# Kernel optimization log

Hardware: AMD Instinct MI355X
Metric: run time of the kernel (lower is better)

Reference implementation:

```python
import jax, jax.numpy as jnp
import numpy as np

EMBED_DIM, KQ_DIM, V_DIM = 512, 64, 64
B, S = 2, 4096

def setup_inputs() -> dict:
    key = jax.random.key(0)
    k1, k2, k3, k4 = jax.random.split(key, 4)
    X = jax.random.normal(k1, (B, S, EMBED_DIM), dtype=jnp.float32)
    # nn.Linear(in, out, bias=False) weight has shape (out, in); y = x @ W.T
    Wq = jax.random.normal(k2, (KQ_DIM, EMBED_DIM), dtype=jnp.float32) * (EMBED_DIM ** -0.5)
    Wk = jax.random.normal(k3, (KQ_DIM, EMBED_DIM), dtype=jnp.float32) * (EMBED_DIM ** -0.5)
    Wv = jax.random.normal(k4, (V_DIM, EMBED_DIM), dtype=jnp.float32) * (EMBED_DIM ** -0.5)
    return {"X": X, "Wq": Wq, "Wk": Wk, "Wv": Wv}

def reference(X, Wq, Wk, Wv):
    # Q,K: [B,S,kq], V: [B,S,v]
    Q = jnp.einsum('bse,ke->bsk', X, Wq)
    K = jnp.einsum('bse,ke->bsk', X, Wk)
    V = jnp.einsum('bse,ve->bsv', X, Wv)
    scores = jnp.einsum('bqk,bsk->bqs', Q, K)  # [B,S,S]
    # FAITHFUL quirk: original divides by kq_dim**(-0.5) == multiply by sqrt(kq_dim)
    scaled = scores / (KQ_DIM ** -0.5)
    attn = jax.nn.softmax(scaled, axis=-1)
    context = jnp.einsum('bqs,bsv->bqv', attn, V)  # [B,S,v]
    return context
```

## Files before the change

### kernel.cpp

```cpp
#include <hip/hip_runtime.h>
#include <hip/hip_bf16.h>


typedef float  f32x16 __attribute__((ext_vector_type(16)));
typedef short  v8bf   __attribute__((ext_vector_type(8)));
typedef int    v4i    __attribute__((ext_vector_type(4)));

#define MFMA32(a, b, c) __builtin_amdgcn_mfma_f32_32x32x16_bf16((a), (b), (c), 0, 0, 0)

union Frag { v4i i4; v8bf b8; unsigned u[4]; };

__device__ __forceinline__ unsigned short f2bf(float x) {
    unsigned u = __float_as_uint(x);
    return (unsigned short)((u + 0x7fffu + ((u >> 16) & 1u)) >> 16);
}
__device__ __forceinline__ float bf2f(unsigned short h) {
    return __uint_as_float(((unsigned)h) << 16);
}
__device__ __forceinline__ unsigned cvt_pk_bf16(float a, float b) {
    unsigned r;
    asm("v_cvt_pk_bf16_f32 %0, %1, %2" : "=v"(r) : "v"(a), "v"(b));
    return r;
}


__global__ __launch_bounds__(256) void splitW_kernel(
    const float* __restrict__ wq, const float* __restrict__ wk, const float* __restrict__ wv,
    unsigned short* __restrict__ hi, unsigned short* __restrict__ lo)
{
    int i = blockIdx.x * 256 + threadIdx.x;
    int e = i * 4;
    const float* src = (e < 32768) ? wq : (e < 65536) ? wk : wv;
    const float sc = (e < 32768) ? 11.541560327111707f : 1.0f;
    int off = e & 32767;
    float4 v = *reinterpret_cast<const float4*>(src + off);
    v.x *= sc; v.y *= sc; v.z *= sc; v.w *= sc;
    unsigned short h0 = f2bf(v.x), h1 = f2bf(v.y), h2 = f2bf(v.z), h3 = f2bf(v.w);
    unsigned short l0 = f2bf(v.x - bf2f(h0)), l1 = f2bf(v.y - bf2f(h1));
    unsigned short l2 = f2bf(v.z - bf2f(h2)), l3 = f2bf(v.w - bf2f(h3));
    reinterpret_cast<uint2*>(hi)[i] =
        make_uint2((unsigned)h0 | ((unsigned)h1 << 16), (unsigned)h2 | ((unsigned)h3 << 16));
    reinterpret_cast<uint2*>(lo)[i] =
        make_uint2((unsigned)l0 | ((unsigned)l1 << 16), (unsigned)l2 | ((unsigned)l3 << 16));
}


__global__ __launch_bounds__(384, 1) void proj_kernel(
    const float* __restrict__ X,
    const unsigned short* __restrict__ Whi, const unsigned short* __restrict__ Wlo,
    unsigned short* __restrict__ Qhi, unsigned short* __restrict__ Qlo,
    unsigned short* __restrict__ Khi, unsigned short* __restrict__ Klo,
    unsigned short* __restrict__ VT)
{
    __shared__ uint4 XhiS[2048];
    __shared__ uint4 XloS[2048];
    __shared__ float t4[4][32][33];

    const int tid = threadIdx.x;
    const int w = tid >> 6;
    const int l = tid & 63, h = l >> 5, r32 = l & 31;
    const int row0 = blockIdx.x * 32;
    const int g = w >> 1, ct = w & 1;

    for (int id = tid; id < 2048; id += 384) {
        const int row = id >> 6, cc = id & 63;
        const float* xp = X + (row0 + row) * 512 + cc * 8;
        float4 va = *reinterpret_cast<const float4*>(xp);
        float4 vb = *reinterpret_cast<const float4*>(xp + 4);
        float xs[8] = {va.x, va.y, va.z, va.w, vb.x, vb.y, vb.z, vb.w};
        unsigned uh[4], ul[4];
#pragma unroll
        for (int j = 0; j < 4; ++j) {
            unsigned short h0 = f2bf(xs[2 * j]),            h1 = f2bf(xs[2 * j + 1]);
            unsigned short l0 = f2bf(xs[2 * j] - bf2f(h0)), l1 = f2bf(xs[2 * j + 1] - bf2f(h1));
            uh[j] = (unsigned)h0 | ((unsigned)h1 << 16);
            ul[j] = (unsigned)l0 | ((unsigned)l1 << 16);
        }
        const int idx = row * 64 + (cc ^ (row & 7));
        XhiS[idx] = make_uint4(uh[0], uh[1], uh[2], uh[3]);
        XloS[idx] = make_uint4(ul[0], ul[1], ul[2], ul[3]);
    }
    __syncthreads();

    f32x16 a0;
#pragma unroll
    for (int r = 0; r < 16; ++r) a0[r] = 0.f;

    for (int kc = 0; kc < 32; ++kc) {
        const int k0 = kc * 16 + 8 * h;
        const int idx = r32 * 64 + ((kc * 2 + h) ^ (r32 & 7));
        Frag xh, b0h;
        xh.i4 = *reinterpret_cast<const v4i*>(&XhiS[idx]);
        const int w0 = (g * 64 + ct * 32 + r32) * 512 + k0;
        b0h.i4 = *reinterpret_cast<const v4i*>(Whi + w0);
        a0 = MFMA32(xh.b8, b0h.b8, a0);
        if (g < 2) {
            Frag xl, b0l;
            xl.i4 = *reinterpret_cast<const v4i*>(&XloS[idx]);
            b0l.i4 = *reinterpret_cast<const v4i*>(Wlo + w0);
            a0 = MFMA32(xh.b8, b0l.b8, a0);
            a0 = MFMA32(xl.b8, b0h.b8, a0);
        }
    }

    const int bb = row0 >> 12;
    const int tl = (row0 & 4095) >> 5;

    if (g < 2) {
#pragma unroll
        for (int u = 0; u < 16; ++u)
            t4[w][(u & 3) + 8 * (u >> 2) + 4 * h][r32] = a0[u];
    }
    __syncthreads();

    if (g == 2) {
#pragma unroll
        for (int c = 0; c < 2; ++c)
#pragma unroll
            for (int hp = 0; hp < 2; ++hp) {
                unsigned p0 = (unsigned)f2bf(a0[8*c + 4*hp + 0]) |
                              ((unsigned)f2bf(a0[8*c + 4*hp + 1]) << 16);
                unsigned p1 = (unsigned)f2bf(a0[8*c + 4*hp + 2]) |
                              ((unsigned)f2bf(a0[8*c + 4*hp + 3]) << 16);
                const int off = ((((bb*128 + tl)*2 + c)*2 + ct)*64 + 32*hp + r32)*8 + 4*h;
                *reinterpret_cast<uint2*>(VT + off) = make_uint2(p0, p1);
            }
    } else if (g == 0) {
        unsigned wh[8], wl[8];
#pragma unroll
        for (int j = 0; j < 8; ++j) {
            float x0 = t4[w][r32][16 * h + 2 * j];
            float x1 = t4[w][r32][16 * h + 2 * j + 1];
            unsigned short h0 = f2bf(x0), h1 = f2bf(x1);
            unsigned short l0 = f2bf(x0 - bf2f(h0)), l1 = f2bf(x1 - bf2f(h1));
            wh[j] = (unsigned)h0 | ((unsigned)h1 << 16);
            wl[j] = (unsigned)l0 | ((unsigned)l1 << 16);
        }
        const int off = (row0 + r32) * 64 + ct * 32 + 16 * h;
        *reinterpret_cast<uint4*>(Qhi + off)     = make_uint4(wh[0], wh[1], wh[2], wh[3]);
        *reinterpret_cast<uint4*>(Qhi + off + 8) = make_uint4(wh[4], wh[5], wh[6], wh[7]);
        *reinterpret_cast<uint4*>(Qlo + off)     = make_uint4(wl[0], wl[1], wl[2], wl[3]);
        *reinterpret_cast<uint4*>(Qlo + off + 8) = make_uint4(wl[4], wl[5], wl[6], wl[7]);
    } else {
        const int dc = ct * 2 + h;
#pragma unroll
        for (int hp = 0; hp < 2; ++hp) {
            unsigned wh[4], wl[4];
#pragma unroll
            for (int jj = 0; jj < 4; ++jj) {
                float x0 = t4[w][r32][16 * h + 8 * hp + 2 * jj];
                float x1 = t4[w][r32][16 * h + 8 * hp + 2 * jj + 1];
                unsigned short h0 = f2bf(x0), h1 = f2bf(x1);
                unsigned short l0 = f2bf(x0 - bf2f(h0)), l1 = f2bf(x1 - bf2f(h1));
                wh[jj] = (unsigned)h0 | ((unsigned)h1 << 16);
                wl[jj] = (unsigned)l0 | ((unsigned)l1 << 16);
            }
            const int off = (((bb*128 + tl)*4 + dc)*64 + 32*hp + r32)*8;
            *reinterpret_cast<uint4*>(Khi + off) = make_uint4(wh[0], wh[1], wh[2], wh[3]);
            *reinterpret_cast<uint4*>(Klo + off) = make_uint4(wl[0], wl[1], wl[2], wl[3]);
        }
    }
}


__global__ __launch_bounds__(256, 3) void attn_kernel(
    const unsigned short* __restrict__ Qhi, const unsigned short* __restrict__ Qlo,
    const unsigned short* __restrict__ Khi, const unsigned short* __restrict__ Klo,
    const unsigned short* __restrict__ VT,
    float* __restrict__ Opart, float* __restrict__ ml)
{
    __shared__ unsigned char RAW[49152];
    auto S  = reinterpret_cast<unsigned short(*)[3][4096]>(RAW);
    auto sO = reinterpret_cast<float(*)[32][68]>(RAW);

    const int tid = threadIdx.x;
    const int w = tid >> 6;
    const int l = tid & 63;
    const int h = l >> 5;
    const int q = l & 31;
    const int bx = blockIdx.x;
    const int b  = bx >> 5;
    const int ks = blockIdx.y;
    const int rowg0 = bx * 128 + w * 32;

    Frag qh[4], ql[4];
#pragma unroll
    for (int dc = 0; dc < 4; ++dc) {
        const int o = (rowg0 + q) * 64 + dc * 16 + 8 * h;
        qh[dc].i4 = *reinterpret_cast<const v4i*>(Qhi + o);
        ql[dc].i4 = *reinterpret_cast<const v4i*>(Qlo + o);
    }

    f32x16 o0, o1;
#pragma unroll
    for (int r = 0; r < 16; ++r) { o0[r] = 0.f; o1[r] = 0.f; }
    float m_run = -1e30f, l_run = 0.f;

    const size_t tb0 = ((size_t)(b * 128 + ks * 16)) * 2048;

    uint4 rgA0, rgA1, rgB0, rgB1, rgC0, rgC1;
    {
        const size_t s = tb0 + (size_t)tid * 8;
        rgA0 = *reinterpret_cast<const uint4*>(Khi + s);
        rgA1 = *reinterpret_cast<const uint4*>(Khi + s + 2048);
        rgB0 = *reinterpret_cast<const uint4*>(Klo + s);
        rgB1 = *reinterpret_cast<const uint4*>(Klo + s + 2048);
        rgC0 = *reinterpret_cast<const uint4*>(VT + s);
        rgC1 = *reinterpret_cast<const uint4*>(VT + s + 2048);
        *reinterpret_cast<uint4*>(&S[0][0][tid * 8])        = rgA0;
        *reinterpret_cast<uint4*>(&S[0][0][tid * 8 + 2048]) = rgA1;
        *reinterpret_cast<uint4*>(&S[0][1][tid * 8])        = rgB0;
        *reinterpret_cast<uint4*>(&S[0][1][tid * 8 + 2048]) = rgB1;
        *reinterpret_cast<uint4*>(&S[0][2][tid * 8])        = rgC0;
        *reinterpret_cast<uint4*>(&S[0][2][tid * 8 + 2048]) = rgC1;
    }
    __syncthreads();

    for (int it = 0; it < 8; ++it) {
        const int cur = it & 1;
        if (it < 7) {
            const size_t s = tb0 + (size_t)(it + 1) * 4096 + (size_t)tid * 8;
            rgA0 = *reinterpret_cast<const uint4*>(Khi + s);
            rgA1 = *reinterpret_cast<const uint4*>(Khi + s + 2048);
            rgB0 = *reinterpret_cast<const uint4*>(Klo + s);
            rgB1 = *reinterpret_cast<const uint4*>(Klo + s + 2048);
            rgC0 = *reinterpret_cast<const uint4*>(VT + s);
            rgC1 = *reinterpret_cast<const uint4*>(VT + s + 2048);
        }

        f32x16 sA, sB;
#pragma unroll
        for (int r = 0; r < 16; ++r) { sA[r] = 0.f; sB[r] = 0.f; }
#pragma unroll
        for (int dc = 0; dc < 4; ++dc) {
            Frag kha, kla, khb, klb;
            kha.i4 = *reinterpret_cast<const v4i*>(&S[cur][0][dc * 512 + l * 8]);
            khb.i4 = *reinterpret_cast<const v4i*>(&S[cur][0][2048 + dc * 512 + l * 8]);
            kla.i4 = *reinterpret_cast<const v4i*>(&S[cur][1][dc * 512 + l * 8]);
            klb.i4 = *reinterpret_cast<const v4i*>(&S[cur][1][2048 + dc * 512 + l * 8]);
            sA = MFMA32(kha.b8, qh[dc].b8, sA);
            sB = MFMA32(khb.b8, qh[dc].b8, sB);
            sA = MFMA32(kha.b8, ql[dc].b8, sA);
            sB = MFMA32(khb.b8, ql[dc].b8, sB);
            sA = MFMA32(kla.b8, qh[dc].b8, sA);
            sB = MFMA32(klb.b8, qh[dc].b8, sB);
        }

        float mb;
        {
            float t[8];
#pragma unroll
            for (int jj = 0; jj < 4; ++jj) {
                t[jj]     = fmaxf(fmaxf(sA[4 * jj], sA[4 * jj + 1]),
                                  fmaxf(sA[4 * jj + 2], sA[4 * jj + 3]));
                t[4 + jj] = fmaxf(fmaxf(sB[4 * jj], sB[4 * jj + 1]),
                                  fmaxf(sB[4 * jj + 2], sB[4 * jj + 3]));
            }
            float u0 = fmaxf(fmaxf(t[0], t[1]), fmaxf(t[2], t[3]));
            float u1 = fmaxf(fmaxf(t[4], t[5]), fmaxf(t[6], t[7]));
            mb = fmaxf(u0, u1);
        }
        mb = fmaxf(mb, __shfl_xor(mb, 32));

        if (!__all(mb <= m_run + 8.f)) {
            const float m_new = fmaxf(m_run, mb);
            const float f = exp2f(m_run - m_new);
#pragma unroll
            for (int r = 0; r < 16; ++r) { o0[r] *= f; o1[r] *= f; }
            l_run *= f;
            m_run = m_new;
        }

        float p[32];
        float ps0 = 0.f, ps1 = 0.f, ps2 = 0.f, ps3 = 0.f;
#pragma unroll
        for (int r = 0; r < 16; r += 4) {
            p[r]      = exp2f(sA[r]     - m_run); ps0 += p[r];
            p[r + 1]  = exp2f(sA[r + 1] - m_run); ps1 += p[r + 1];
            p[r + 2]  = exp2f(sA[r + 2] - m_run); ps2 += p[r + 2];
            p[r + 3]  = exp2f(sA[r + 3] - m_run); ps3 += p[r + 3];
            p[16 + r]     = exp2f(sB[r]     - m_run); ps0 += p[16 + r];
            p[16 + r + 1] = exp2f(sB[r + 1] - m_run); ps1 += p[16 + r + 1];
            p[16 + r + 2] = exp2f(sB[r + 2] - m_run); ps2 += p[16 + r + 2];
            p[16 + r + 3] = exp2f(sB[r + 3] - m_run); ps3 += p[16 + r + 3];
        }
        float ps = (ps0 + ps1) + (ps2 + ps3);
        ps += __shfl_xor(ps, 32);
        l_run += ps;

        unsigned U[16];
#pragma unroll
        for (int j = 0; j < 8; ++j) {
            U[j]     = cvt_pk_bf16(p[2 * j],      p[2 * j + 1]);
            U[8 + j] = cvt_pk_bf16(p[16 + 2 * j], p[16 + 2 * j + 1]);
        }
        unsigned tA0 = h ? U[0]  : U[2];
        unsigned tA1 = h ? U[1]  : U[3];
        unsigned tA2 = h ? U[4]  : U[6];
        unsigned tA3 = h ? U[5]  : U[7];
        unsigned tB0 = h ? U[8]  : U[10];
        unsigned tB1 = h ? U[9]  : U[11];
        unsigned tB2 = h ? U[12] : U[14];
        unsigned tB3 = h ? U[13] : U[15];
        unsigned rA0 = __shfl_xor(tA0, 32);
        unsigned rA1 = __shfl_xor(tA1, 32);
        unsigned rA2 = __shfl_xor(tA2, 32);
        unsigned rA3 = __shfl_xor(tA3, 32);
        unsigned rB0 = __shfl_xor(tB0, 32);
        unsigned rB1 = __shfl_xor(tB1, 32);
        unsigned rB2 = __shfl_xor(tB2, 32);
        unsigned rB3 = __shfl_xor(tB3, 32);
        Frag p0f, p1f, p2f, p3f;
        if (h == 0) {
            p0f.u[0] = U[0];  p0f.u[1] = U[1];  p0f.u[2] = rA0;   p0f.u[3] = rA1;
            p1f.u[0] = U[4];  p1f.u[1] = U[5];  p1f.u[2] = rA2;   p1f.u[3] = rA3;
            p2f.u[0] = U[8];  p2f.u[1] = U[9];  p2f.u[2] = rB0;   p2f.u[3] = rB1;
            p3f.u[0] = U[12]; p3f.u[1] = U[13]; p3f.u[2] = rB2;   p3f.u[3] = rB3;
        } else {
            p0f.u[0] = rA0;   p0f.u[1] = rA1;   p0f.u[2] = U[2];  p0f.u[3] = U[3];
            p1f.u[0] = rA2;   p1f.u[1] = rA3;   p1f.u[2] = U[6];  p1f.u[3] = U[7];
            p2f.u[0] = rB0;   p2f.u[1] = rB1;   p2f.u[2] = U[10]; p2f.u[3] = U[11];
            p3f.u[0] = rB2;   p3f.u[1] = rB3;   p3f.u[2] = U[14]; p3f.u[3] = U[15];
        }

#pragma unroll
        for (int tb = 0; tb < 2; ++tb) {
#pragma unroll
            for (int c = 0; c < 2; ++c) {
                const Frag& pf = tb ? (c ? p3f : p2f) : (c ? p1f : p0f);
#pragma unroll
                for (int vc = 0; vc < 2; ++vc) {
                    Frag vf;
                    vf.i4 = *reinterpret_cast<const v4i*>(
                        &S[cur][2][tb * 2048 + (c * 2 + vc) * 512 + l * 8]);
                    if (vc == 0) o0 = MFMA32(vf.b8, pf.b8, o0);
                    else         o1 = MFMA32(vf.b8, pf.b8, o1);
                }
            }
        }

        if (it < 7) {
            const int nxt = cur ^ 1;
            *reinterpret_cast<uint4*>(&S[nxt][0][tid * 8])        = rgA0;
            *reinterpret_cast<uint4*>(&S[nxt][0][tid * 8 + 2048]) = rgA1;
            *reinterpret_cast<uint4*>(&S[nxt][1][tid * 8])        = rgB0;
            *reinterpret_cast<uint4*>(&S[nxt][1][tid * 8 + 2048]) = rgB1;
            *reinterpret_cast<uint4*>(&S[nxt][2][tid * 8])        = rgC0;
            *reinterpret_cast<uint4*>(&S[nxt][2][tid * 8 + 2048]) = rgC1;
        }
        __syncthreads();
    }

    if (h == 0) {
        const int rowg = rowg0 + q;
        *reinterpret_cast<float2*>(&ml[((size_t)ks * 8192 + rowg) * 2]) =
            make_float2(m_run, l_run);
    }
#pragma unroll
    for (int vc = 0; vc < 2; ++vc) {
        const f32x16& a = vc ? o1 : o0;
#pragma unroll
        for (int u = 0; u < 4; ++u) {
            float4 v4 = make_float4(a[4 * u], a[4 * u + 1], a[4 * u + 2], a[4 * u + 3]);
            *reinterpret_cast<float4*>(&sO[w][q][vc * 32 + 8 * u + 4 * h]) = v4;
        }
    }
    __syncthreads();

#pragma unroll
    for (int k = 0; k < 8; ++k) {
        const int f = tid + k * 256;
        const int rl = f >> 4;
        const int v4 = f & 15;
        float4 val = *reinterpret_cast<const float4*>(&sO[rl >> 5][rl & 31][v4 * 4]);
        *reinterpret_cast<float4*>(
            &Opart[(((size_t)ks * 8192) + bx * 128 + rl) * 64 + v4 * 4]) = val;
    }
}

__global__ __launch_bounds__(256) void merge_kernel(
    const float* __restrict__ Opart, const float* __restrict__ ml, float* __restrict__ out)
{
    const int idx = blockIdx.x * 256 + threadIdx.x;
    const int row = idx >> 4, vb = (idx & 15) * 4;
    float mv[8], lv[8];
    float ms = -1e30f;
#pragma unroll
    for (int s = 0; s < 8; ++s) {
        float2 m2 = *reinterpret_cast<const float2*>(&ml[((size_t)s * 8192 + row) * 2]);
        mv[s] = m2.x; lv[s] = m2.y;
        ms = fmaxf(ms, m2.x);
    }
    float L = 0.f;
    float a0 = 0.f, a1 = 0.f, a2 = 0.f, a3 = 0.f;
#pragma unroll
    for (int s = 0; s < 8; ++s) {
        const float fw = exp2f(mv[s] - ms);
        L += fw * lv[s];
        float4 a = *reinterpret_cast<const float4*>(
            &Opart[((size_t)s * 8192 + row) * 64 + vb]);
        a0 += fw * a.x; a1 += fw * a.y; a2 += fw * a.z; a3 += fw * a.w;
    }
    const float inv = 1.0f / L;
    *reinterpret_cast<float4*>(out + (size_t)row * 64 + vb) =
        make_float4(a0 * inv, a1 * inv, a2 * inv, a3 * inv);
}


extern "C" void kernel_launch(void* const* d_in, const int* in_sizes, int n_in,
                              void* d_out, int out_size, void* d_ws, size_t ws_size,
                              hipStream_t stream)
{
    const float* X  = (const float*)d_in[0];
    const float* Wq = (const float*)d_in[1];
    const float* Wk = (const float*)d_in[2];
    const float* Wv = (const float*)d_in[3];
    float* out = (float*)d_out;

    unsigned short* Qhi = (unsigned short*)d_ws;
    unsigned short* Qlo = Qhi + 524288;
    unsigned short* Khi = Qlo + 524288;
    unsigned short* Klo = Khi + 524288;
    unsigned short* VT  = Klo + 524288;
    unsigned short* Whi = VT + 524288;
    unsigned short* Wlo = Whi + 98304;
    float* Opart = (float*)Whi;
    float* ml    = Opart + 4194304;

    splitW_kernel<<<96, 256, 0, stream>>>(Wq, Wk, Wv, Whi, Wlo);
    proj_kernel<<<256, 384, 0, stream>>>(X, Whi, Wlo, Qhi, Qlo, Khi, Klo, VT);
    attn_kernel<<<dim3(64, 8), 256, 0, stream>>>(Qhi, Qlo, Khi, Klo, VT, Opart, ml);
    merge_kernel<<<512, 256, 0, stream>>>(Opart, ml, out);
}
```

Before: 58.32 us.

## Use per-half local max for exp and store split-K partials as bf16

The softmax exponentials are now computed against each half-wave's local block maximum, so they no longer wait on the cross-half shuffle and the running-max update. The result is rescaled to the running max afterwards through per-half scale factors applied at bf16 packing and in the row sum. Separately, the split-K partial outputs are written to the workspace as bf16 instead of fp32, and the merge kernel reads them back. This halves partial-output traffic at the cost of extra multiplies and reduced precision in the partials.

```diff
diff --git a/kernel.cpp b/kernel.cpp
--- a/kernel.cpp
+++ b/kernel.cpp
@@ -167,7 +167,7 @@
     const unsigned short* __restrict__ Qhi, const unsigned short* __restrict__ Qlo,
     const unsigned short* __restrict__ Khi, const unsigned short* __restrict__ Klo,
     const unsigned short* __restrict__ VT,
-    float* __restrict__ Opart, float* __restrict__ ml)
+    unsigned short* __restrict__ Opart, float* __restrict__ ml)
 {
     __shared__ unsigned char RAW[49152];
     auto S  = reinterpret_cast<unsigned short(*)[3][4096]>(RAW);
@@ -246,7 +246,7 @@
             sB = MFMA32(klb.b8, qh[dc].b8, sB);
         }
 
-        float mb;
+        float mbh;
         {
             float t[8];
 #pragma unroll
@@ -258,41 +258,44 @@
             }
             float u0 = fmaxf(fmaxf(t[0], t[1]), fmaxf(t[2], t[3]));
             float u1 = fmaxf(fmaxf(t[4], t[5]), fmaxf(t[6], t[7]));
-            mb = fmaxf(u0, u1);
-        }
-        mb = fmaxf(mb, __shfl_xor(mb, 32));
-
-        if (!__all(mb <= m_run + 8.f)) {
-            const float m_new = fmaxf(m_run, mb);
+            mbh = fmaxf(u0, u1);
+        }
+        const float mbo = __shfl_xor(mbh, 32);
+
+        float p[32];
+        float ps0 = 0.f, ps1 = 0.f, ps2 = 0.f, ps3 = 0.f;
+#pragma unroll
+        for (int r = 0; r < 16; r += 4) {
+            p[r]      = exp2f(sA[r]     - mbh); ps0 += p[r];
+            p[r + 1]  = exp2f(sA[r + 1] - mbh); ps1 += p[r + 1];
+            p[r + 2]  = exp2f(sA[r + 2] - mbh); ps2 += p[r + 2];
+            p[r + 3]  = exp2f(sA[r + 3] - mbh); ps3 += p[r + 3];
+            p[16 + r]     = exp2f(sB[r]     - mbh); ps0 += p[16 + r];
+            p[16 + r + 1] = exp2f(sB[r + 1] - mbh); ps1 += p[16 + r + 1];
+            p[16 + r + 2] = exp2f(sB[r + 2] - mbh); ps2 += p[16 + r + 2];
+            p[16 + r + 3] = exp2f(sB[r + 3] - mbh); ps3 += p[16 + r + 3];
+        }
+        const float psh = (ps0 + ps1) + (ps2 + ps3);
+        const float pso = __shfl_xor(psh, 32);
+
+        const float mb_all = fmaxf(mbh, mbo);
+        if (!__all(mb_all <= m_run + 8.f)) {
+            const float m_new = fmaxf(m_run, mb_all);
             const float f = exp2f(m_run - m_new);
 #pragma unroll
             for (int r = 0; r < 16; ++r) { o0[r] *= f; o1[r] *= f; }
             l_run *= f;
             m_run = m_new;
         }
-
-        float p[32];
-        float ps0 = 0.f, ps1 = 0.f, ps2 = 0.f, ps3 = 0.f;
-#pragma unroll
-        for (int r = 0; r < 16; r += 4) {
-            p[r]      = exp2f(sA[r]     - m_run); ps0 += p[r];
-            p[r + 1]  = exp2f(sA[r + 1] - m_run); ps1 += p[r + 1];
-            p[r + 2]  = exp2f(sA[r + 2] - m_run); ps2 += p[r + 2];
-            p[r + 3]  = exp2f(sA[r + 3] - m_run); ps3 += p[r + 3];
-            p[16 + r]     = exp2f(sB[r]     - m_run); ps0 += p[16 + r];
-            p[16 + r + 1] = exp2f(sB[r + 1] - m_run); ps1 += p[16 + r + 1];
-            p[16 + r + 2] = exp2f(sB[r + 2] - m_run); ps2 += p[16 + r + 2];
-            p[16 + r + 3] = exp2f(sB[r + 3] - m_run); ps3 += p[16 + r + 3];
-        }
-        float ps = (ps0 + ps1) + (ps2 + ps3);
-        ps += __shfl_xor(ps, 32);
-        l_run += ps;
+        const float sh = exp2f(mbh - m_run);
+        const float so = exp2f(mbo - m_run);
+        l_run += psh * sh + pso * so;
 
         unsigned U[16];
 #pragma unroll
         for (int j = 0; j < 8; ++j) {
-            U[j]     = cvt_pk_bf16(p[2 * j],      p[2 * j + 1]);
-            U[8 + j] = cvt_pk_bf16(p[16 + 2 * j], p[16 + 2 * j + 1]);
+            U[j]     = cvt_pk_bf16(p[2 * j] * sh,      p[2 * j + 1] * sh);
+            U[8 + j] = cvt_pk_bf16(p[16 + 2 * j] * sh, p[16 + 2 * j + 1] * sh);
         }
         unsigned tA0 = h ? U[0]  : U[2];
         unsigned tA1 = h ? U[1]  : U[3];
@@ -373,13 +376,17 @@
         const int rl = f >> 4;
         const int v4 = f & 15;
         float4 val = *reinterpret_cast<const float4*>(&sO[rl >> 5][rl & 31][v4 * 4]);
-        *reinterpret_cast<float4*>(
-            &Opart[(((size_t)ks * 8192) + bx * 128 + rl) * 64 + v4 * 4]) = val;
+        unsigned u0 = (unsigned)f2bf(val.x) | ((unsigned)f2bf(val.y) << 16);
+        unsigned u1 = (unsigned)f2bf(val.z) | ((unsigned)f2bf(val.w) << 16);
+        *reinterpret_cast<uint2*>(
+            &Opart[(((size_t)ks * 8192) + bx * 128 + rl) * 64 + v4 * 4]) =
+            make_uint2(u0, u1);
     }
 }
 
 __global__ __launch_bounds__(256) void merge_kernel(
-    const float* __restrict__ Opart, const float* __restrict__ ml, float* __restrict__ out)
+    const unsigned short* __restrict__ Opart, const float* __restrict__ ml,
+    float* __restrict__ out)
 {
     const int idx = blockIdx.x * 256 + threadIdx.x;
     const int row = idx >> 4, vb = (idx & 15) * 4;
@@ -397,9 +404,12 @@
     for (int s = 0; s < 8; ++s) {
         const float fw = exp2f(mv[s] - ms);
         L += fw * lv[s];
-        float4 a = *reinterpret_cast<const float4*>(
+        uint2 a = *reinterpret_cast<const uint2*>(
             &Opart[((size_t)s * 8192 + row) * 64 + vb]);
-        a0 += fw * a.x; a1 += fw * a.y; a2 += fw * a.z; a3 += fw * a.w;
+        a0 += fw * bf2f((unsigned short)(a.x & 0xffff));
+        a1 += fw * bf2f((unsigned short)(a.x >> 16));
+        a2 += fw * bf2f((unsigned short)(a.y & 0xffff));
+        a3 += fw * bf2f((unsigned short)(a.y >> 16));
     }
     const float inv = 1.0f / L;
     *reinterpret_cast<float4*>(out + (size_t)row * 64 + vb) =
@@ -424,8 +434,8 @@
     unsigned short* VT  = Klo + 524288;
     unsigned short* Whi = VT + 524288;
     unsigned short* Wlo = Whi + 98304;
-    float* Opart = (float*)Whi;
-    float* ml    = Opart + 4194304;
+    unsigned short* Opart = Whi;
+    float* ml = (float*)(Opart + 4194304);
 
     splitW_kernel<<<96, 256, 0, stream>>>(Wq, Wk, Wv, Whi, Wlo);
     proj_kernel<<<256, 384, 0, stream>>>(X, Whi, Wlo, Qhi, Qlo, Khi, Klo, VT);
```

Result: no change. 59.27 us (+1.6%).
